# Performance work log

Hardware: AMD Instinct MI355X
Metric: run time of the kernel (lower is better)

The kernel has to match this reference:

```python
import jax, jax.numpy as jnp
import numpy as np

B, N, F, D, H, L, K = 128, 128, 13, 256, 8, 8, 10
FF = 2 * D  # FFN / hidden width
HEAD = D // H


def setup_inputs() -> dict:
    key = jax.random.key(0)
    ks = iter(jax.random.split(key, 64))
    def nrm(shape, scale=0.02):
        return jax.random.normal(next(ks), shape, dtype=jnp.float32) * scale
    return {
        "input_features": jax.random.normal(next(ks), (B, N, F), dtype=jnp.float32),
        "input_points": jax.random.normal(next(ks), (B, N, 2), dtype=jnp.float32),
        "input_mask": jnp.ones((B, N, 1), dtype=jnp.float32),
        "input_time": jax.random.uniform(next(ks), (B, 1), dtype=jnp.float32),
        # get_encoding: Dense(2D, gelu) -> Dense(D, gelu)
        "enc_w1": nrm((F, FF)), "enc_b1": jnp.zeros((FF,), jnp.float32),
        "enc_w2": nrm((FF, D)), "enc_b2": jnp.zeros((D,), jnp.float32),
        # FourierProjection MLP (no bias, swish)
        "four_w1": nrm((D, FF)), "four_w2": nrm((FF, D)),
        # FiLM time projection (no bias)
        "time_w": nrm((D, FF)),
        # local KNN MLPs: round 0 input 2*F, round 1 input 2*D
        "loc1_w1": nrm((2 * F, FF)), "loc1_b1": jnp.zeros((FF,), jnp.float32),
        "loc1_w2": nrm((FF, D)), "loc1_b2": jnp.zeros((D,), jnp.float32),
        "loc2_w1": nrm((2 * D, FF)), "loc2_b1": jnp.zeros((FF,), jnp.float32),
        "loc2_w2": nrm((FF, D)), "loc2_b2": jnp.zeros((D,), jnp.float32),
        # transformer encoder layers, stacked over L
        "qkv_w": nrm((L, D, 3 * D)), "qkv_b": jnp.zeros((L, 3 * D), jnp.float32),
        "out_w": nrm((L, D, D)), "out_b": jnp.zeros((L, D), jnp.float32),
        "ln1_g": jnp.ones((L, D), jnp.float32), "ln1_b": jnp.zeros((L, D), jnp.float32),
        "ff1_w": nrm((L, D, FF)), "ff1_b": jnp.zeros((L, FF), jnp.float32),
        "ff2_w": nrm((L, FF, D)), "ff2_b": jnp.zeros((L, D), jnp.float32),
        "gamma": jnp.full((L, D), 1e-5, dtype=jnp.float32),
        "ln2_g": jnp.ones((L, D), jnp.float32), "ln2_b": jnp.zeros((L, D), jnp.float32),
    }


def _ln(x, g, b, eps=1e-5):
    m = jnp.mean(x, axis=-1, keepdims=True)
    v = jnp.var(x, axis=-1, keepdims=True)
    return (x - m) * jax.lax.rsqrt(v + eps) * g + b


def _fourier(t, w1, w2):
    # t: (B,1) -> (B,D)
    half = D // 2
    emb = np.log(10000.0) / (half - 1)
    freq = jnp.exp(-emb * jnp.arange(half, dtype=jnp.float32))
    angle = t * freq[None, :] * 1000.0  # (B, half)
    e = jnp.concatenate([jnp.sin(angle), jnp.cos(angle)], axis=-1)
    e = jax.nn.silu(e @ w1)
    return jax.nn.silu(e @ w2)


def _get_neighbors(points, feats, w1, b1, w2, b2):
    # points: (B,N,P), feats: (B,N,C) -> (B,N,D)
    r = jnp.sum(points * points, axis=-1)  # (B,N)
    d = r[:, :, None] - 2.0 * jnp.einsum('bnp,bmp->bnm', points, points) + r[:, None, :]
    _, idx = jax.lax.top_k(-d, K + 1)
    idx = idx[:, :, 1:]  # drop self, (B,N,K)
    knn = jax.vmap(lambda f, i: f[i])(feats, idx)  # (B,N,K,C)
    center = jnp.broadcast_to(feats[:, :, None, :], knn.shape)
    local = jnp.concatenate([knn - center, center], axis=-1)  # (B,N,K,2C)
    local = jax.nn.gelu(local @ w1 + b1)
    local = jax.nn.gelu(local @ w2 + b2)
    return jnp.mean(local, axis=2)


def _mha(x, mask, wqkv, bqkv, wo, bo):
    Bx, Nx, _ = x.shape
    qkv = x @ wqkv + bqkv
    q, k, v = jnp.split(qkv, 3, axis=-1)
    def heads(t):
        return t.reshape(Bx, Nx, H, HEAD).transpose(0, 2, 1, 3)
    q, k, v = heads(q), heads(k), heads(v)
    scores = jnp.einsum('bhqd,bhkd->bhqk', q, k) * (1.0 / np.sqrt(HEAD))
    keep = mask[:, None, None, :, 0] > 0  # (B,1,1,N)
    scores = jnp.where(keep, scores, -1e9)
    a = jax.nn.softmax(scores, axis=-1)
    o = jnp.einsum('bhqk,bhkd->bhqd', a, v).transpose(0, 2, 1, 3).reshape(Bx, Nx, D)
    return o @ wo + bo


def _pet(input_features, input_points, input_mask, input_time,
         enc_w1, enc_b1, enc_w2, enc_b2, four_w1, four_w2, time_w,
         loc1_w1, loc1_b1, loc1_w2, loc1_b2, loc2_w1, loc2_b1, loc2_w2, loc2_b2,
         qkv_w, qkv_b, out_w, out_b, ln1_g, ln1_b, ff1_w, ff1_b, ff2_w, ff2_b,
         gamma, ln2_g, ln2_b):
    # feature encoding (RandomDrop is identity at eval / feature_drop=0)
    enc = jax.nn.gelu(input_features @ enc_w1 + enc_b1)
    enc = jax.nn.gelu(enc @ enc_w2 + enc_b2)  # (B,N,D)
    # FiLM time conditioning
    t = _fourier(input_time, four_w1, four_w2)  # (B,D)
    t = t[:, None, :] * input_mask  # (B,N,D)
    scale, shift = jnp.split(t @ time_w, 2, axis=-1)
    enc = enc * (1.0 + scale) + shift
    # local KNN aggregation
    coord_shift = 999.0 * (1.0 - input_mask)  # (B,N,1)
    points = input_points[:, :, :2]
    lf = _get_neighbors(coord_shift + points, input_features, loc1_w1, loc1_b1, loc1_w2, loc1_b2)
    lf = _get_neighbors(coord_shift + lf, lf, loc2_w1, loc2_b1, loc2_w2, loc2_b2)
    enc = enc + lf
    skip = enc
    x = enc
    for i in range(L):
        res = x
        a = _mha(x, input_mask, qkv_w[i], qkv_b[i], out_w[i], out_b[i])
        x = _ln(res + a, ln1_g[i], ln1_b[i])
        res = x
        h = jax.nn.gelu(x @ ff1_w[i] + ff1_b[i])
        h = h @ ff2_w[i] + ff2_b[i]
        h = h * gamma[i] * input_mask  # LayerScale with mask
        x = _ln(res + h, ln2_g[i], ln2_b[i])
    return x + skip


def reference(input_features, input_points, input_mask, input_time,
              enc_w1, enc_b1, enc_w2, enc_b2, four_w1, four_w2, time_w,
              loc1_w1, loc1_b1, loc1_w2, loc1_b2, loc2_w1, loc2_b1, loc2_w2, loc2_b2,
              qkv_w, qkv_b, out_w, out_b, ln1_g, ln1_b, ff1_w, ff1_b, ff2_w, ff2_b,
              gamma, ln2_g, ln2_b):
    return _pet(input_features, input_points, input_mask, input_time,
                enc_w1, enc_b1, enc_w2, enc_b2, four_w1, four_w2, time_w,
                loc1_w1, loc1_b1, loc1_w2, loc1_b2, loc2_w1, loc2_b1, loc2_w2, loc2_b2,
                qkv_w, qkv_b, out_w, out_b, ln1_g, ln1_b, ff1_w, ff1_b, ff2_w, ff2_b,
                gamma, ln2_g, ln2_b)
```

## Files before the change

kernel.cpp:

```cpp
#include <hip/hip_runtime.h>
#include <hip/hip_bf16.h>
#include <cmath>

#define DEV_INLINE __device__ __forceinline__

constexpr int Bn = 128;
constexpr int Nn = 128;
constexpr int Fn = 13;
constexpr int Dn = 256;
constexpr int Ln = 8;
constexpr int Kn = 10;
constexpr int FFn = 512;
constexpr int Tn = Bn * Nn;
constexpr int Rn = Tn * Kn;

typedef __attribute__((ext_vector_type(4))) float f32x4;
typedef __attribute__((ext_vector_type(8))) short bf16x8;
typedef unsigned short us;

__device__ float g_x[Tn * Dn];
__device__ float g_skip[Tn * Dn];
__device__ float g_big[Tn * Dn];
__device__ float g_u[Bn * FFn];
__device__ float g_r[Tn];
__device__ float g_pqbias[2048];
__device__ int   g_idx[Rn];
__device__ us g_bigb[Tn * 768];
__device__ us g_xb[Tn * Dn];
__device__ us g_attb[Tn * Dn];
__device__ us g_lf1b[Tn * Dn];
__device__ us g_pq[Tn * 1024];
__device__ us g_h2b[Rn * Dn];
__device__ us g_feat16[Tn * 32];
constexpr int OFF_ENC1 = 0;
constexpr int OFF_ENC2 = OFF_ENC1 + 512 * 32;
constexpr int OFF_W2A  = OFF_ENC2 + 256 * 512;
constexpr int OFF_W2B  = OFF_W2A + 256 * 512;
constexpr int OFF_PQ1  = OFF_W2B + 256 * 512;
constexpr int OFF_PQ2  = OFF_PQ1 + 1024 * 32;
constexpr int OFF_QKV  = OFF_PQ2 + 1024 * 256;
constexpr int OFF_OUT  = OFF_QKV + 8 * 768 * 256;
constexpr int OFF_FF1  = OFF_OUT + 8 * 256 * 256;
constexpr int OFF_FF2  = OFF_FF1 + 8 * 512 * 256;
constexpr int WT_TOTAL = OFF_FF2 + 8 * 256 * 512;
__device__ us g_wt[WT_TOTAL];

DEV_INLINE float gelu_f(float x) {
    float x2 = x * x;
    float m = x * fmaf(x2, -0.07135537f, -1.59576912f);
    float t = __expf(m);
    return x * __builtin_amdgcn_rcpf(1.f + t);
}
DEV_INLINE us f2b(float x) {
    __hip_bfloat16 h = __float2bfloat16(x);
    return *(us*)&h;
}
DEV_INLINE float blo(unsigned u) { return __uint_as_float(u << 16); }
DEV_INLINE float bhi(unsigned u) { return __uint_as_float(u & 0xFFFF0000u); }
DEV_INLINE unsigned pk2(float a, float b) {
    float2 f; f.x = a; f.y = b;
    __hip_bfloat162 h = __float22bfloat162_rn(f);
    return *(unsigned*)&h;
}

#define GLOAD16(gp, lp)                                                            \
    __builtin_amdgcn_global_load_lds(                                              \
        (const __attribute__((address_space(1))) unsigned int*)(gp),               \
        (__attribute__((address_space(3))) unsigned int*)(lp), 16, 0, 0)

constexpr int UP0 = 0;
constexpr int UP1 = UP0 + 16;
constexpr int UP2 = UP1 + 128;
constexpr int UP3 = UP2 + 128;
constexpr int UP4 = UP3 + 128;
constexpr int UP5 = UP4 + 1536;
constexpr int UP6 = UP5 + 512;
constexpr int UP7 = UP6 + 1024;
constexpr int UP8 = UP7 + 1024;
constexpr int UP9 = UP8 + 1024;
constexpr int UP10 = UP9 + 1024;
constexpr int UP11 = UP10 + 2048;
constexpr int UP12 = UP11 + 128;
constexpr int UPN = UP12 + 128;

DEV_INLINE void prep_seg(const float* __restrict__ src, us* __restrict__ dst,
                         int Kreal, int Kpad, int Nd, long sstride, long dstride,
                         int gx, int gy, int lb, int tid, float* tile) {
    int z = lb / (gx * gy);
    int rem = lb - z * gx * gy;
    int by = rem / gx, bx = rem - by * gx;
    const float* s = src + (size_t)z * sstride;
    us* d = dst + (size_t)z * dstride;
    int cn = tid & 31, rk = tid >> 5;
    int kbase = by * 32, nbase = bx * 32;
#pragma unroll
    for (int p = 0; p < 4; p++) {
        int k = kbase + p * 8 + rk;
        float v = (k < Kreal) ? s[(size_t)k * Nd + nbase + cn] : 0.f;
        tile[(p * 8 + rk) * 33 + cn] = v;
    }
    __syncthreads();
#pragma unroll
    for (int p = 0; p < 4; p++) {
        int nl = p * 8 + rk;
        d[(size_t)(nbase + nl) * Kpad + kbase + cn] = f2b(tile[cn * 33 + nl]);
    }
}

DEV_INLINE void prepPQ_seg(const float* __restrict__ w1, const float* __restrict__ b1,
                           us* __restrict__ dst, float* __restrict__ bdst,
                           int Kreal, int Kpad, int n, int tid) {
    for (int k = tid; k < Kpad; k += 256) {
        float v;
        if (n < 512) v = (k < Kreal) ? w1[(size_t)k * 512 + n] : 0.f;
        else {
            int m = n - 512;
            v = (k < Kreal) ? (w1[(size_t)(Kreal + k) * 512 + m] - w1[(size_t)k * 512 + m]) : 0.f;
        }
        dst[(size_t)n * Kpad + k] = f2b(v);
    }
    if (tid == 0) bdst[n] = (n < 512) ? 0.f : b1[n - 512];
}

__global__ __launch_bounds__(256) void k_uprep(
    const float* __restrict__ enc_w1, const float* __restrict__ enc_w2,
    const float* __restrict__ l1w2, const float* __restrict__ l2w2,
    const float* __restrict__ qkv_w, const float* __restrict__ out_w,
    const float* __restrict__ ff1w, const float* __restrict__ ff2w,
    const float* __restrict__ l1w1, const float* __restrict__ l1b1,
    const float* __restrict__ l2w1, const float* __restrict__ l2b1,
    const float* __restrict__ feat, const float* __restrict__ tin,
    const float* __restrict__ four_w1, const float* __restrict__ four_w2,
    const float* __restrict__ time_w, const float* __restrict__ pts,
    const float* __restrict__ mask,
    us* __restrict__ wt, float* __restrict__ pqbias, us* __restrict__ fp,
    float* __restrict__ u, int* __restrict__ idx) {
    __shared__ float shmem[1056];
    int b = blockIdx.x, tid = threadIdx.x;
    if (b < UP1) {
        prep_seg(enc_w1, wt + OFF_ENC1, 13, 32, 512, 0, 0, 16, 1, b - UP0, tid, shmem);
    } else if (b < UP2) {
        prep_seg(enc_w2, wt + OFF_ENC2, 512, 512, 256, 0, 0, 8, 16, b - UP1, tid, shmem);
    } else if (b < UP3) {
        prep_seg(l1w2, wt + OFF_W2A, 512, 512, 256, 0, 0, 8, 16, b - UP2, tid, shmem);
    } else if (b < UP4) {
        prep_seg(l2w2, wt + OFF_W2B, 512, 512, 256, 0, 0, 8, 16, b - UP3, tid, shmem);
    } else if (b < UP5) {
        prep_seg(qkv_w, wt + OFF_QKV, 256, 256, 768, 256 * 768, 768 * 256, 24, 8, b - UP4, tid, shmem);
    } else if (b < UP6) {
        prep_seg(out_w, wt + OFF_OUT, 256, 256, 256, 256 * 256, 256 * 256, 8, 8, b - UP5, tid, shmem);
    } else if (b < UP7) {
        prep_seg(ff1w, wt + OFF_FF1, 256, 256, 512, 256 * 512, 512 * 256, 16, 8, b - UP6, tid, shmem);
    } else if (b < UP8) {
        prep_seg(ff2w, wt + OFF_FF2, 512, 512, 256, 512 * 256, 256 * 512, 8, 16, b - UP7, tid, shmem);
    } else if (b < UP9) {
        prepPQ_seg(l1w1, l1b1, wt + OFF_PQ1, pqbias, 13, 32, b - UP8, tid);
    } else if (b < UP10) {
        prepPQ_seg(l2w1, l2b1, wt + OFF_PQ2, pqbias + 1024, 256, 256, b - UP9, tid);
    } else if (b < UP11) {
        int gid = (b - UP10) * 256 + tid;
        int t = gid >> 5, c = gid & 31;
        fp[gid] = (c < Fn) ? f2b(feat[(size_t)t * Fn + c]) : (us)0;
    } else if (b < UP12) {
        float* e = shmem; float* e1 = shmem + 256; float* t2 = shmem + 768;
        int bb = b - UP11;
        float tv = tin[bb];
        if (tid < 128) {
            const float emb = 0.07252236513366287f;
            float fr = expf(-emb * (float)tid);
            float ang = tv * fr * 1000.f;
            e[tid] = sinf(ang);
            e[tid + 128] = cosf(ang);
        }
        __syncthreads();
        for (int j = tid; j < 512; j += 256) {
            float s = 0.f;
            for (int i = 0; i < 256; i++) s += e[i] * four_w1[(size_t)i * 512 + j];
            e1[j] = s / (1.f + expf(-s));
        }
        __syncthreads();
        {
            float s = 0.f;
            for (int i = 0; i < 512; i++) s += e1[i] * four_w2[(size_t)i * 256 + tid];
            t2[tid] = s / (1.f + expf(-s));
        }
        __syncthreads();
        for (int j = tid; j < 512; j += 256) {
            float s = 0.f;
            for (int i = 0; i < 256; i++) s += t2[i] * time_w[(size_t)i * 512 + j];
            u[(size_t)bb * 512 + j] = s;
        }
    } else {
        float* px = shmem; float* py = shmem + 128; float* rr = shmem + 256;
        int bb = b - UP12;
        if (tid < 128) {
            int n = tid;
            float shift = 999.f * (1.f - mask[bb * Nn + n]);
            float x = pts[(size_t)(bb * Nn + n) * 2 + 0] + shift;
            float y = pts[(size_t)(bb * Nn + n) * 2 + 1] + shift;
            px[n] = x; py[n] = y; rr[n] = x * x + y * y;
        }
        __syncthreads();
        if (tid < 128) {
            int n = tid;
            float x = px[n], y = py[n], rn = rr[n];
            float bd[Kn + 1]; int bi[Kn + 1];
#pragma unroll
            for (int j = 0; j <= Kn; j++) { bd[j] = 3.4e38f; bi[j] = -1; }
            for (int m = 0; m < Nn; m++) {
                float d = rn - 2.f * (x * px[m] + y * py[m]) + rr[m];
                if (d < bd[Kn]) {
                    int j = Kn;
                    while (j > 0 && d < bd[j - 1]) { bd[j] = bd[j - 1]; bi[j] = bi[j - 1]; j--; }
                    bd[j] = d; bi[j] = m;
                }
            }
            for (int j = 1; j <= Kn; j++) idx[(size_t)(bb * Nn + n) * Kn + j - 1] = bi[j];
        }
    }
}

template <int EPI, bool OBF>
__global__ __launch_bounds__(256) void k_mg2(const us* __restrict__ A,
                                             const us* __restrict__ Bt,
                                             const float* __restrict__ bias,
                                             void* __restrict__ Cp,
                                             int Kd, int Nd) {
    __shared__ __align__(16) us As[128 * 32];
    __shared__ __align__(16) us Bs[128 * 32];
    int tid = threadIdx.x;
    int m0 = blockIdx.y << 7, n0 = blockIdx.x << 7;
    int wave = tid >> 6, lane = tid & 63;
    int wm = (wave & 1) << 6, wn = (wave >> 1) << 6;
    int lm = lane & 15, quad = lane >> 4;
    int r0 = (wave << 5) + (lane >> 2);
    int colu = (((lane & 3) ^ ((lane >> 2) & 3)) << 3);
    const us* pa0 = A + (size_t)(m0 + r0) * Kd + colu;
    const us* pa1 = A + (size_t)(m0 + r0 + 16) * Kd + colu;
    const us* pb0 = Bt + (size_t)(n0 + r0) * Kd + colu;
    const us* pb1 = Bt + (size_t)(n0 + r0 + 16) * Kd + colu;
    auto lAs = (__attribute__((address_space(3))) us*)As;
    auto lBs = (__attribute__((address_space(3))) us*)Bs;
    int lbase = wave << 10;
    int fcol = ((quad ^ (lm & 3)) << 3);
    f32x4 acc[4][4] = {};
    for (int k0 = 0; k0 < Kd; k0 += 32) {
        __syncthreads();
        GLOAD16(pa0 + k0, lAs + lbase);
        GLOAD16(pa1 + k0, lAs + lbase + 512);
        GLOAD16(pb0 + k0, lBs + lbase);
        GLOAD16(pb1 + k0, lBs + lbase + 512);
        __syncthreads();
        bf16x8 afr[4], bfr[4];
#pragma unroll
        for (int i = 0; i < 4; i++) {
            afr[i] = *(const bf16x8*)&As[(wm + i * 16 + lm) * 32 + fcol];
            bfr[i] = *(const bf16x8*)&Bs[(wn + i * 16 + lm) * 32 + fcol];
        }
#pragma unroll
        for (int mf = 0; mf < 4; mf++)
#pragma unroll
            for (int nf = 0; nf < 4; nf++)
                acc[mf][nf] = __builtin_amdgcn_mfma_f32_16x16x32_bf16(afr[mf], bfr[nf], acc[mf][nf], 0, 0, 0);
    }
    float bvs[4];
#pragma unroll
    for (int nf = 0; nf < 4; nf++) bvs[nf] = bias[n0 + wn + nf * 16 + lm];
#pragma unroll
    for (int mf = 0; mf < 4; mf++) {
#pragma unroll
        for (int r = 0; r < 4; r++) {
            size_t row = (size_t)(m0 + wm + mf * 16 + (quad << 2) + r);
#pragma unroll
            for (int nf = 0; nf < 4; nf++) {
                float v = acc[mf][nf][r] + bvs[nf];
                if (EPI == 1) v = gelu_f(v);
                size_t ci = row * Nd + n0 + wn + nf * 16 + lm;
                if constexpr (OBF) ((us*)Cp)[ci] = f2b(v);
                else ((float*)Cp)[ci] = v;
            }
        }
    }
}

template <bool PM, bool FINAL>
__global__ __launch_bounds__(512) void k_mgln(const us* __restrict__ A,
                                              const us* __restrict__ Bt,
                                              const float* __restrict__ bias,
                                              const float* __restrict__ res,
                                              const float* __restrict__ gamma,
                                              const float* __restrict__ mask,
                                              const float* __restrict__ lng,
                                              const float* __restrict__ lnb,
                                              const float* __restrict__ skip,
                                              float* __restrict__ xout,
                                              us* __restrict__ xbout,
                                              float* __restrict__ finout,
                                              int Kd) {
    __shared__ __align__(16) us As[128 * 32];
    __shared__ __align__(16) us Bs[256 * 32];
    __shared__ float2 part[4][128];
    __shared__ float2 stat[128];
    int tid = threadIdx.x;
    int m0 = blockIdx.x << 7;
    int wave = tid >> 6, lane = tid & 63;
    int wm = (wave & 1) << 6, wn = (wave >> 1) << 6;
    int grp = wave >> 1;
    int lm = lane & 15, quad = lane >> 4;
    int ar = (wave << 4) + (lane >> 2);
    int br = (wave << 5) + (lane >> 2);
    int colu = (((lane & 3) ^ ((lane >> 2) & 3)) << 3);
    const us* pa = A + (size_t)(m0 + ar) * Kd + colu;
    const us* pb0 = Bt + (size_t)br * Kd + colu;
    const us* pb1 = Bt + (size_t)(br + 16) * Kd + colu;
    auto lAs = (__attribute__((address_space(3))) us*)As;
    auto lBs = (__attribute__((address_space(3))) us*)Bs;
    int fcol = ((quad ^ (lm & 3)) << 3);
    f32x4 acc[4][4] = {};
    for (int k0 = 0; k0 < Kd; k0 += 32) {
        __syncthreads();
        GLOAD16(pa + k0, lAs + (wave << 9));
        GLOAD16(pb0 + k0, lBs + (wave << 10));
        GLOAD16(pb1 + k0, lBs + (wave << 10) + 512);
        __syncthreads();
        bf16x8 afr[4], bfr[4];
#pragma unroll
        for (int i = 0; i < 4; i++) {
            afr[i] = *(const bf16x8*)&As[(wm + i * 16 + lm) * 32 + fcol];
            bfr[i] = *(const bf16x8*)&Bs[(wn + i * 16 + lm) * 32 + fcol];
        }
#pragma unroll
        for (int mf = 0; mf < 4; mf++)
#pragma unroll
            for (int nf = 0; nf < 4; nf++)
                acc[mf][nf] = __builtin_amdgcn_mfma_f32_16x16x32_bf16(afr[mf], bfr[nf], acc[mf][nf], 0, 0, 0);
    }
    float bvs[4], gms[4];
#pragma unroll
    for (int nf = 0; nf < 4; nf++) {
        int col = wn + nf * 16 + lm;
        bvs[nf] = bias[col];
        if (PM) gms[nf] = gamma[col];
    }
#pragma unroll
    for (int mf = 0; mf < 4; mf++) {
#pragma unroll
        for (int r = 0; r < 4; r++) {
            int rowl = wm + mf * 16 + (quad << 2) + r;
            size_t row = (size_t)(m0 + rowl);
            float mrow = PM ? mask[row] : 0.f;
            float s1 = 0.f, s2 = 0.f;
#pragma unroll
            for (int nf = 0; nf < 4; nf++) {
                int col = wn + nf * 16 + lm;
                float rv = res[row * 256 + col];
                float v = acc[mf][nf][r] + bvs[nf];
                v = PM ? fmaf(v * gms[nf], mrow, rv) : rv + v;
                acc[mf][nf][r] = v;
                s1 += v; s2 += v * v;
            }
            s1 += __shfl_xor(s1, 1, 64); s2 += __shfl_xor(s2, 1, 64);
            s1 += __shfl_xor(s1, 2, 64); s2 += __shfl_xor(s2, 2, 64);
            s1 += __shfl_xor(s1, 4, 64); s2 += __shfl_xor(s2, 4, 64);
            s1 += __shfl_xor(s1, 8, 64); s2 += __shfl_xor(s2, 8, 64);
            if (lm == 0) { float2 p; p.x = s1; p.y = s2; part[grp][rowl] = p; }
        }
    }
    __syncthreads();
    if (tid < 128) {
        float2 p0 = part[0][tid], p1 = part[1][tid], p2 = part[2][tid], p3 = part[3][tid];
        float s = p0.x + p1.x + p2.x + p3.x;
        float q = p0.y + p1.y + p2.y + p3.y;
        float mean = s * (1.f / 256.f);
        float var = q * (1.f / 256.f) - mean * mean;
        float2 st; st.x = mean; st.y = rsqrtf(var + 1e-5f);
        stat[tid] = st;
    }
    __syncthreads();
    float gvs[4], bts[4];
#pragma unroll
    for (int nf = 0; nf < 4; nf++) {
        int col = wn + nf * 16 + lm;
        gvs[nf] = lng[col];
        bts[nf] = lnb[col];
    }
#pragma unroll
    for (int mf = 0; mf < 4; mf++) {
#pragma unroll
        for (int r = 0; r < 4; r++) {
            int rowl = wm + mf * 16 + (quad << 2) + r;
            size_t row = (size_t)(m0 + rowl);
            float2 st = stat[rowl];
#pragma unroll
            for (int nf = 0; nf < 4; nf++) {
                int col = wn + nf * 16 + lm;
                float nv = fmaf((acc[mf][nf][r] - st.x) * st.y, gvs[nf], bts[nf]);
                xout[row * 256 + col] = nv;
                xbout[row * 256 + col] = f2b(nv);
                if (FINAL) finout[row * 256 + col] = nv + skip[row * 256 + col];
            }
        }
    }
}

__global__ __launch_bounds__(512) void k_knng(const us* __restrict__ pq,
                                              const int* __restrict__ idx,
                                              const us* __restrict__ Bt,
                                              const float* __restrict__ bias,
                                              us* __restrict__ h2b) {
    __shared__ __align__(16) us As[128 * 64];
    __shared__ __align__(16) us Bs[256 * 64];
    int tid = threadIdx.x;
    int m0 = blockIdx.x << 7;
    int wave = tid >> 6, lane = tid & 63;
    int wm = (wave & 1) << 6, wn = (wave >> 1) << 6;
    int lm = lane & 15, quad = lane >> 4;
    int arow = tid >> 2, acolu = (tid & 3) << 4;
    int asw = arow & 7;
    int ablk0 = ((tid & 3) << 1) ^ asw, ablk1 = (((tid & 3) << 1) + 1) ^ asw;
    int r = m0 + arow;
    int tok = r / 10;
    int nb = idx[r];
    int prow = (tok & ~127) + nb;
    const us* Pp = pq + (size_t)prow * 1024 + acolu;
    const us* Qp = pq + (size_t)tok * 1024 + 512 + acolu;
    int brow = (wave << 5) + (lane >> 3);
    int bcol = (((lane & 7) ^ (lane >> 3)) << 3);
    const us* pb = Bt + (size_t)brow * 512 + bcol;
    auto lBs = (__attribute__((address_space(3))) us*)Bs;
    int lbase = wave << 11;
    int fsw = lm & 7;
    f32x4 acc[4][4] = {};
    for (int k0 = 0; k0 < 512; k0 += 64) {
        uint4 pv0 = *(const uint4*)(Pp + k0);
        uint4 pv1 = *(const uint4*)(Pp + k0 + 8);
        uint4 qv0 = *(const uint4*)(Qp + k0);
        uint4 qv1 = *(const uint4*)(Qp + k0 + 8);
        uint4 h0, h1;
        h0.x = pk2(gelu_f(blo(pv0.x) + blo(qv0.x)), gelu_f(bhi(pv0.x) + bhi(qv0.x)));
        h0.y = pk2(gelu_f(blo(pv0.y) + blo(qv0.y)), gelu_f(bhi(pv0.y) + bhi(qv0.y)));
        h0.z = pk2(gelu_f(blo(pv0.z) + blo(qv0.z)), gelu_f(bhi(pv0.z) + bhi(qv0.z)));
        h0.w = pk2(gelu_f(blo(pv0.w) + blo(qv0.w)), gelu_f(bhi(pv0.w) + bhi(qv0.w)));
        h1.x = pk2(gelu_f(blo(pv1.x) + blo(qv1.x)), gelu_f(bhi(pv1.x) + bhi(qv1.x)));
        h1.y = pk2(gelu_f(blo(pv1.y) + blo(qv1.y)), gelu_f(bhi(pv1.y) + bhi(qv1.y)));
        h1.z = pk2(gelu_f(blo(pv1.z) + blo(qv1.z)), gelu_f(bhi(pv1.z) + bhi(qv1.z)));
        h1.w = pk2(gelu_f(blo(pv1.w) + blo(qv1.w)), gelu_f(bhi(pv1.w) + bhi(qv1.w)));
        __syncthreads();
        GLOAD16(pb + k0, lBs + lbase);
        GLOAD16(pb + k0 + 8 * 512, lBs + lbase + 512);
        GLOAD16(pb + k0 + 16 * 512, lBs + lbase + 1024);
        GLOAD16(pb + k0 + 24 * 512, lBs + lbase + 1536);
        *(uint4*)&As[arow * 64 + (ablk0 << 3)] = h0;
        *(uint4*)&As[arow * 64 + (ablk1 << 3)] = h1;
        __syncthreads();
#pragma unroll
        for (int sub = 0; sub < 2; sub++) {
            int lblk = (sub << 2) + quad;
            int fcol = ((lblk ^ fsw) << 3);
            bf16x8 afr[4], bfr[4];
#pragma unroll
            for (int i = 0; i < 4; i++) {
                afr[i] = *(const bf16x8*)&As[(wm + i * 16 + lm) * 64 + fcol];
                bfr[i] = *(const bf16x8*)&Bs[(wn + i * 16 + lm) * 64 + fcol];
            }
#pragma unroll
            for (int mf = 0; mf < 4; mf++)
#pragma unroll
                for (int nf = 0; nf < 4; nf++)
                    acc[mf][nf] = __builtin_amdgcn_mfma_f32_16x16x32_bf16(afr[mf], bfr[nf], acc[mf][nf], 0, 0, 0);
        }
    }
    float bvs[4];
#pragma unroll
    for (int nf = 0; nf < 4; nf++) bvs[nf] = bias[wn + nf * 16 + lm];
#pragma unroll
    for (int mf = 0; mf < 4; mf++) {
#pragma unroll
        for (int rr = 0; rr < 4; rr++) {
            size_t row = (size_t)(m0 + wm + mf * 16 + (quad << 2) + rr);
#pragma unroll
            for (int nf = 0; nf < 4; nf++) {
                float v = gelu_f(acc[mf][nf][rr] + bvs[nf]);
                h2b[row * 256 + wn + nf * 16 + lm] = f2b(v);
            }
        }
    }
}

__global__ __launch_bounds__(64) void k_mean1s(const us* __restrict__ h2b,
                                               const float* __restrict__ mask,
                                               us* __restrict__ lfb,
                                               float* __restrict__ big,
                                               float* __restrict__ r) {
    int t = blockIdx.x, lane = threadIdx.x;
    int c = lane << 2;
    const us* p = h2b + (size_t)t * Kn * 256 + c;
    float s0 = 0.f, s1 = 0.f, s2 = 0.f, s3 = 0.f;
#pragma unroll
    for (int k = 0; k < Kn; k++) {
        uint2 v = *(const uint2*)(p + k * 256);
        s0 += blo(v.x); s1 += bhi(v.x);
        s2 += blo(v.y); s3 += bhi(v.y);
    }
    s0 *= 0.1f; s1 *= 0.1f; s2 *= 0.1f; s3 *= 0.1f;
    uint2 ob; ob.x = pk2(s0, s1); ob.y = pk2(s2, s3);
    *(uint2*)&lfb[(size_t)t * 256 + c] = ob;
    float sh = 999.f * (1.f - mask[t]);
    float4 w; w.x = s0 + sh; w.y = s1 + sh; w.z = s2 + sh; w.w = s3 + sh;
    *(float4*)&big[(size_t)t * 256 + c] = w;
    float sq = w.x * w.x + w.y * w.y + w.z * w.z + w.w * w.w;
#pragma unroll
    for (int off = 32; off; off >>= 1) sq += __shfl_xor(sq, off, 64);
    if (lane == 0) r[t] = sq;
}

__global__ __launch_bounds__(256) void k_dtop(const float* __restrict__ big,
                                              const float* __restrict__ r,
                                              int* __restrict__ idx) {
    __shared__ float Dm[128][132];
    __shared__ float At[16][132];
    int b = blockIdx.x, tid = threadIdx.x;
    int tx = tid & 15, ty = tid >> 4;
    const float* A = big + (size_t)b * Nn * Dn;
    float acc[8][8] = {};
    int srow = tid >> 1, sc8 = (tid & 1) << 3;
    for (int k0 = 0; k0 < 256; k0 += 16) {
        float4 v0 = *(const float4*)&A[(size_t)srow * 256 + k0 + sc8];
        float4 v1 = *(const float4*)&A[(size_t)srow * 256 + k0 + sc8 + 4];
        __syncthreads();
        At[sc8 + 0][srow] = v0.x; At[sc8 + 1][srow] = v0.y;
        At[sc8 + 2][srow] = v0.z; At[sc8 + 3][srow] = v0.w;
        At[sc8 + 4][srow] = v1.x; At[sc8 + 5][srow] = v1.y;
        At[sc8 + 6][srow] = v1.z; At[sc8 + 7][srow] = v1.w;
        __syncthreads();
#pragma unroll
        for (int kk = 0; kk < 16; kk++) {
            float av[8], bv[8];
#pragma unroll
            for (int i = 0; i < 8; i++) av[i] = At[kk][ty * 8 + i];
#pragma unroll
            for (int j = 0; j < 8; j++) bv[j] = At[kk][tx * 8 + j];
#pragma unroll
            for (int i = 0; i < 8; i++)
#pragma unroll
                for (int j = 0; j < 8; j++) acc[i][j] += av[i] * bv[j];
        }
    }
    __syncthreads();
#pragma unroll
    for (int i = 0; i < 8; i++) {
        int n = ty * 8 + i;
        float rn = r[b * Nn + n];
#pragma unroll
        for (int j = 0; j < 8; j++) {
            int m = tx * 8 + j;
            Dm[n][m] = rn - 2.f * acc[i][j] + r[b * Nn + m];
        }
    }
    __syncthreads();
    if (tid < 128) {
        int n = tid;
        float bd[Kn + 1]; int bi[Kn + 1];
#pragma unroll
        for (int j = 0; j <= Kn; j++) { bd[j] = 3.4e38f; bi[j] = -1; }
        for (int m = 0; m < Nn; m++) {
            float d = Dm[n][m];
            if (d < bd[Kn]) {
                int j = Kn;
                while (j > 0 && d < bd[j - 1]) { bd[j] = bd[j - 1]; bi[j] = bi[j - 1]; j--; }
                bd[j] = d; bi[j] = m;
            }
        }
        for (int j = 1; j <= Kn; j++) idx[(size_t)(b * Nn + n) * Kn + j - 1] = bi[j];
    }
}

__global__ __launch_bounds__(256) void k_meanc(const us* __restrict__ h2b,
                                               const float* __restrict__ u,
                                               const float* __restrict__ mask,
                                               float* __restrict__ x,
                                               float* __restrict__ skip,
                                               us* __restrict__ xb) {
    int t = blockIdx.x, c = threadIdx.x;
    const us* p = h2b + (size_t)t * Kn * 256 + c;
    float s = 0.f;
#pragma unroll
    for (int k = 0; k < Kn; k++) s += blo((unsigned)p[k * 256]);
    s *= 0.1f;
    int b = t >> 7;
    float m = mask[t];
    float xv = x[(size_t)t * Dn + c];
    float sc = u[(size_t)b * 512 + c];
    float sh = u[(size_t)b * 512 + 256 + c];
    float v = xv * (1.f + m * sc) + m * sh + s;
    x[(size_t)t * Dn + c] = v;
    skip[(size_t)t * Dn + c] = v;
    xb[(size_t)t * Dn + c] = f2b(v);
}

__global__ __launch_bounds__(256) void k_attn(const us* __restrict__ qkv,
                                              const float* __restrict__ mask,
                                              us* __restrict__ outp) {
    __shared__ __align__(16) us Qs[128 * 40];
    __shared__ __align__(16) us Ks[128 * 40];
    __shared__ __align__(16) us Vt[32 * 136];
    __shared__ __align__(16) us Ps[128 * 136];
    __shared__ float msk[128];
    int bh = blockIdx.x;
    int b = bh >> 3, h = bh & 7;
    int tid = threadIdx.x;
    int wave = tid >> 6, lane = tid & 63;
    int lm = lane & 15, quad = lane >> 4;
    int wm = wave << 5;
    {
        int row = tid >> 1, off = (tid & 1) << 4;
        const us* rp = qkv + (size_t)(b * 128 + row) * 768 + h * 32 + off;
        *(uint4*)&Qs[row * 40 + off] = *(const uint4*)(rp);
        *(uint4*)&Qs[row * 40 + off + 8] = *(const uint4*)(rp + 8);
        *(uint4*)&Ks[row * 40 + off] = *(const uint4*)(rp + 256);
        *(uint4*)&Ks[row * 40 + off + 8] = *(const uint4*)(rp + 264);
        union { uint4 u[2]; us s[16]; } tv;
        tv.u[0] = *(const uint4*)(rp + 512);
        tv.u[1] = *(const uint4*)(rp + 520);
#pragma unroll
        for (int j = 0; j < 16; j++) Vt[(off + j) * 136 + row] = tv.s[j];
        if (tid < 128) msk[tid] = mask[b * 128 + tid];
    }
    __syncthreads();
    f32x4 acc[2][8] = {};
    {
        bf16x8 aq[2];
#pragma unroll
        for (int mf = 0; mf < 2; mf++)
            aq[mf] = *(const bf16x8*)&Qs[(wm + mf * 16 + lm) * 40 + (quad << 3)];
#pragma unroll
        for (int nf = 0; nf < 8; nf++) {
            bf16x8 bk = *(const bf16x8*)&Ks[(nf * 16 + lm) * 40 + (quad << 3)];
            acc[0][nf] = __builtin_amdgcn_mfma_f32_16x16x32_bf16(aq[0], bk, acc[0][nf], 0, 0, 0);
            acc[1][nf] = __builtin_amdgcn_mfma_f32_16x16x32_bf16(aq[1], bk, acc[1][nf], 0, 0, 0);
        }
    }
    {
        const float sc = 0.17677669529663687f;
        float mkc[8];
#pragma unroll
        for (int nf = 0; nf < 8; nf++) mkc[nf] = msk[nf * 16 + lm];
#pragma unroll
        for (int mf = 0; mf < 2; mf++) {
#pragma unroll
            for (int nf = 0; nf < 8; nf++)
#pragma unroll
                for (int r = 0; r < 4; r++) {
                    float s = acc[mf][nf][r];
                    acc[mf][nf][r] = mkc[nf] > 0.f ? s * sc : -1.0e9f;
                }
#pragma unroll
            for (int r = 0; r < 4; r++) {
                float m = acc[mf][0][r];
#pragma unroll
                for (int nf = 1; nf < 8; nf++) m = fmaxf(m, acc[mf][nf][r]);
                m = fmaxf(m, __shfl_xor(m, 1, 64));
                m = fmaxf(m, __shfl_xor(m, 2, 64));
                m = fmaxf(m, __shfl_xor(m, 4, 64));
                m = fmaxf(m, __shfl_xor(m, 8, 64));
                float s = 0.f;
#pragma unroll
                for (int nf = 0; nf < 8; nf++) {
                    float p = __expf(acc[mf][nf][r] - m);
                    acc[mf][nf][r] = p;
                    s += p;
                }
                s += __shfl_xor(s, 1, 64);
                s += __shfl_xor(s, 2, 64);
                s += __shfl_xor(s, 4, 64);
                s += __shfl_xor(s, 8, 64);
                float linv = __builtin_amdgcn_rcpf(s);
                int prow = wm + mf * 16 + (quad << 2) + r;
#pragma unroll
                for (int nf = 0; nf < 8; nf++)
                    Ps[prow * 136 + nf * 16 + lm] = f2b(acc[mf][nf][r] * linv);
            }
        }
    }
    __syncthreads();
    f32x4 oacc[2][2] = {};
    for (int kt = 0; kt < 4; kt++) {
        bf16x8 ap[2], bv[2];
#pragma unroll
        for (int mf = 0; mf < 2; mf++)
            ap[mf] = *(const bf16x8*)&Ps[(wm + mf * 16 + lm) * 136 + kt * 32 + (quad << 3)];
#pragma unroll
        for (int nf = 0; nf < 2; nf++)
            bv[nf] = *(const bf16x8*)&Vt[(nf * 16 + lm) * 136 + kt * 32 + (quad << 3)];
#pragma unroll
        for (int mf = 0; mf < 2; mf++)
#pragma unroll
            for (int nf = 0; nf < 2; nf++)
                oacc[mf][nf] = __builtin_amdgcn_mfma_f32_16x16x32_bf16(ap[mf], bv[nf], oacc[mf][nf], 0, 0, 0);
    }
#pragma unroll
    for (int mf = 0; mf < 2; mf++)
#pragma unroll
        for (int r = 0; r < 4; r++) {
            int row = wm + mf * 16 + (quad << 2) + r;
#pragma unroll
            for (int nf = 0; nf < 2; nf++)
                outp[(size_t)(b * 128 + row) * 256 + h * 32 + nf * 16 + lm] = f2b(oacc[mf][nf][r]);
        }
}

extern "C" void kernel_launch(void* const* d_in, const int* in_sizes, int n_in,
                              void* d_out, int out_size, void* d_ws, size_t ws_size,
                              hipStream_t stream) {
    (void)in_sizes; (void)n_in; (void)out_size; (void)d_ws; (void)ws_size;
    const float* f_feat = (const float*)d_in[0];
    const float* f_pts  = (const float*)d_in[1];
    const float* f_mask = (const float*)d_in[2];
    const float* f_time = (const float*)d_in[3];
    const float* enc_w1 = (const float*)d_in[4];
    const float* enc_b1 = (const float*)d_in[5];
    const float* enc_w2 = (const float*)d_in[6];
    const float* enc_b2 = (const float*)d_in[7];
    const float* four_w1 = (const float*)d_in[8];
    const float* four_w2 = (const float*)d_in[9];
    const float* time_w = (const float*)d_in[10];
    const float* l1w1 = (const float*)d_in[11];
    const float* l1b1 = (const float*)d_in[12];
    const float* l1w2 = (const float*)d_in[13];
    const float* l1b2 = (const float*)d_in[14];
    const float* l2w1 = (const float*)d_in[15];
    const float* l2b1 = (const float*)d_in[16];
    const float* l2w2 = (const float*)d_in[17];
    const float* l2b2 = (const float*)d_in[18];
    const float* qkv_w = (const float*)d_in[19];
    const float* qkv_b = (const float*)d_in[20];
    const float* out_w = (const float*)d_in[21];
    const float* out_b = (const float*)d_in[22];
    const float* ln1g = (const float*)d_in[23];
    const float* ln1b = (const float*)d_in[24];
    const float* ff1w = (const float*)d_in[25];
    const float* ff1b = (const float*)d_in[26];
    const float* ff2w = (const float*)d_in[27];
    const float* ff2b = (const float*)d_in[28];
    const float* gam  = (const float*)d_in[29];
    const float* ln2g = (const float*)d_in[30];
    const float* ln2b = (const float*)d_in[31];
    float* out = (float*)d_out;

    float *x, *skip, *big, *u, *r, *pqbias;
    int* idx;
    us *bigb, *xb, *attb, *lf1b, *pq, *h2b, *feat16, *wt;
    hipGetSymbolAddress((void**)&x,    HIP_SYMBOL(g_x));
    hipGetSymbolAddress((void**)&skip, HIP_SYMBOL(g_skip));
    hipGetSymbolAddress((void**)&big,  HIP_SYMBOL(g_big));
    hipGetSymbolAddress((void**)&u,    HIP_SYMBOL(g_u));
    hipGetSymbolAddress((void**)&r,    HIP_SYMBOL(g_r));
    hipGetSymbolAddress((void**)&pqbias, HIP_SYMBOL(g_pqbias));
    hipGetSymbolAddress((void**)&idx,  HIP_SYMBOL(g_idx));
    hipGetSymbolAddress((void**)&bigb, HIP_SYMBOL(g_bigb));
    hipGetSymbolAddress((void**)&xb,   HIP_SYMBOL(g_xb));
    hipGetSymbolAddress((void**)&attb, HIP_SYMBOL(g_attb));
    hipGetSymbolAddress((void**)&lf1b, HIP_SYMBOL(g_lf1b));
    hipGetSymbolAddress((void**)&pq,   HIP_SYMBOL(g_pq));
    hipGetSymbolAddress((void**)&h2b,  HIP_SYMBOL(g_h2b));
    hipGetSymbolAddress((void**)&feat16, HIP_SYMBOL(g_feat16));
    hipGetSymbolAddress((void**)&wt,   HIP_SYMBOL(g_wt));

    k_uprep<<<UPN, 256, 0, stream>>>(
        enc_w1, enc_w2, l1w2, l2w2, qkv_w, out_w, ff1w, ff2w,
        l1w1, l1b1, l2w1, l2b1, f_feat, f_time, four_w1, four_w2, time_w,
        f_pts, f_mask, wt, pqbias, feat16, u, idx);

    k_mg2<1, true><<<dim3(4, 128), 256, 0, stream>>>(feat16, wt + OFF_ENC1, enc_b1, bigb, 32, 512);
    k_mg2<1, false><<<dim3(2, 128), 256, 0, stream>>>(bigb, wt + OFF_ENC2, enc_b2, x, 512, 256);
    k_mg2<0, true><<<dim3(8, 128), 256, 0, stream>>>(feat16, wt + OFF_PQ1, pqbias, pq, 32, 1024);
    k_knng<<<Rn / 128, 512, 0, stream>>>(pq, idx, wt + OFF_W2A, l1b2, h2b);
    k_mean1s<<<Tn, 64, 0, stream>>>(h2b, f_mask, lf1b, big, r);
    k_dtop<<<Bn, 256, 0, stream>>>(big, r, idx);
    k_mg2<0, true><<<dim3(8, 128), 256, 0, stream>>>(lf1b, wt + OFF_PQ2, pqbias + 1024, pq, 256, 1024);
    k_knng<<<Rn / 128, 512, 0, stream>>>(pq, idx, wt + OFF_W2B, l2b2, h2b);
    k_meanc<<<Tn, 256, 0, stream>>>(h2b, u, f_mask, x, skip, xb);
    for (int l = 0; l < Ln; l++) {
        k_mg2<0, true><<<dim3(6, 128), 256, 0, stream>>>(
            xb, wt + OFF_QKV + (size_t)l * 768 * 256, qkv_b + l * 768, bigb, 256, 768);
        k_attn<<<Bn * 8, 256, 0, stream>>>(bigb, f_mask, attb);
        k_mgln<false, false><<<128, 512, 0, stream>>>(
            attb, wt + OFF_OUT + (size_t)l * 256 * 256, out_b + l * 256,
            x, nullptr, f_mask, ln1g + l * Dn, ln1b + l * Dn, nullptr, x, xb, nullptr, 256);
        k_mg2<1, true><<<dim3(4, 128), 256, 0, stream>>>(
            xb, wt + OFF_FF1 + (size_t)l * 512 * 256, ff1b + l * 512, bigb, 256, 512);
        if (l < Ln - 1)
            k_mgln<true, false><<<128, 512, 0, stream>>>(
                bigb, wt + OFF_FF2 + (size_t)l * 256 * 512, ff2b + l * 256,
                x, gam + l * Dn, f_mask, ln2g + l * Dn, ln2b + l * Dn, nullptr, x, xb, nullptr, 512);
        else
            k_mgln<true, true><<<128, 512, 0, stream>>>(
                bigb, wt + OFF_FF2 + (size_t)l * 256 * 512, ff2b + l * 256,
                x, gam + l * Dn, f_mask, ln2g + l * Dn, ln2b + l * Dn, skip, x, xb, out, 512);
    }
}
```

Baseline: 1.572 ms.

## Keep residual stream in bf16 only and split kNN distance/top-k kernels

The fp32 residual copy of x is removed: the fused GEMM+LayerNorm kernels now read the residual from the bf16 activation buffer and write the normalized result back to it in place. This cuts global memory reads and writes in every layer. In exchange, the residual is rounded to bf16 at each of the 16 LayerNorm stages, which can accumulate error. Separately, the per-batch distance-plus-top-k kernel is split into a tiled distance GEMM spread over more blocks, which writes a global distance matrix, and a separate per-row top-k kernel.

```diff
diff --git a/kernel.cpp b/kernel.cpp
--- a/kernel.cpp
+++ b/kernel.cpp
@@ -21,6 +21,7 @@
 __device__ float g_x[Tn * Dn];
 __device__ float g_skip[Tn * Dn];
 __device__ float g_big[Tn * Dn];
+__device__ float g_dm[Tn * Nn];
 __device__ float g_u[Bn * FFn];
 __device__ float g_r[Tn];
 __device__ float g_pqbias[2048];
@@ -287,13 +288,12 @@
 __global__ __launch_bounds__(512) void k_mgln(const us* __restrict__ A,
                                               const us* __restrict__ Bt,
                                               const float* __restrict__ bias,
-                                              const float* __restrict__ res,
+                                              const us* __restrict__ res,
                                               const float* __restrict__ gamma,
                                               const float* __restrict__ mask,
                                               const float* __restrict__ lng,
                                               const float* __restrict__ lnb,
                                               const float* __restrict__ skip,
-                                              float* __restrict__ xout,
                                               us* __restrict__ xbout,
                                               float* __restrict__ finout,
                                               int Kd) {
@@ -353,7 +353,7 @@
 #pragma unroll
             for (int nf = 0; nf < 4; nf++) {
                 int col = wn + nf * 16 + lm;
-                float rv = res[row * 256 + col];
+                float rv = blo((unsigned)res[row * 256 + col]);
                 float v = acc[mf][nf][r] + bvs[nf];
                 v = PM ? fmaf(v * gms[nf], mrow, rv) : rv + v;
                 acc[mf][nf][r] = v;
@@ -395,9 +395,8 @@
             for (int nf = 0; nf < 4; nf++) {
                 int col = wn + nf * 16 + lm;
                 float nv = fmaf((acc[mf][nf][r] - st.x) * st.y, gvs[nf], bts[nf]);
-                xout[row * 256 + col] = nv;
-                xbout[row * 256 + col] = f2b(nv);
                 if (FINAL) finout[row * 256 + col] = nv + skip[row * 256 + col];
+                else xbout[row * 256 + col] = f2b(nv);
             }
         }
     }
@@ -514,71 +513,70 @@
     if (lane == 0) r[t] = sq;
 }
 
-__global__ __launch_bounds__(256) void k_dtop(const float* __restrict__ big,
+__global__ __launch_bounds__(256) void k_dist(const float* __restrict__ fe,
                                               const float* __restrict__ r,
-                                              int* __restrict__ idx) {
-    __shared__ float Dm[128][132];
-    __shared__ float At[16][132];
-    int b = blockIdx.x, tid = threadIdx.x;
+                                              float* __restrict__ Dm) {
+    int b = blockIdx.z;
+    int m0 = blockIdx.x * 64, n0 = blockIdx.y * 64;
+    const float* A = fe + (size_t)b * Nn * Dn;
+    __shared__ float As[16][68];
+    __shared__ float Bs[16][68];
+    int tid = threadIdx.x;
     int tx = tid & 15, ty = tid >> 4;
-    const float* A = big + (size_t)b * Nn * Dn;
-    float acc[8][8] = {};
-    int srow = tid >> 1, sc8 = (tid & 1) << 3;
-    for (int k0 = 0; k0 < 256; k0 += 16) {
-        float4 v0 = *(const float4*)&A[(size_t)srow * 256 + k0 + sc8];
-        float4 v1 = *(const float4*)&A[(size_t)srow * 256 + k0 + sc8 + 4];
-        __syncthreads();
-        At[sc8 + 0][srow] = v0.x; At[sc8 + 1][srow] = v0.y;
-        At[sc8 + 2][srow] = v0.z; At[sc8 + 3][srow] = v0.w;
-        At[sc8 + 4][srow] = v1.x; At[sc8 + 5][srow] = v1.y;
-        At[sc8 + 6][srow] = v1.z; At[sc8 + 7][srow] = v1.w;
+    int ar = tid >> 2, ac = (tid & 3) << 2;
+    float acc[4][4] = {};
+    for (int k0 = 0; k0 < Dn; k0 += 16) {
+        float4 av = *(const float4*)&A[(size_t)(n0 + ar) * Dn + k0 + ac];
+        float4 bv = *(const float4*)&A[(size_t)(m0 + ar) * Dn + k0 + ac];
+        __syncthreads();
+        As[ac + 0][ar] = av.x; As[ac + 1][ar] = av.y; As[ac + 2][ar] = av.z; As[ac + 3][ar] = av.w;
+        Bs[ac + 0][ar] = bv.x; Bs[ac + 1][ar] = bv.y; Bs[ac + 2][ar] = bv.z; Bs[ac + 3][ar] = bv.w;
         __syncthreads();
 #pragma unroll
         for (int kk = 0; kk < 16; kk++) {
-            float av[8], bv[8];
-#pragma unroll
-            for (int i = 0; i < 8; i++) av[i] = At[kk][ty * 8 + i];
-#pragma unroll
-            for (int j = 0; j < 8; j++) bv[j] = At[kk][tx * 8 + j];
-#pragma unroll
-            for (int i = 0; i < 8; i++)
-#pragma unroll
-                for (int j = 0; j < 8; j++) acc[i][j] += av[i] * bv[j];
-        }
-    }
-    __syncthreads();
-#pragma unroll
-    for (int i = 0; i < 8; i++) {
-        int n = ty * 8 + i;
+            float4 a = *(const float4*)&As[kk][ty << 2];
+            float4 b2 = *(const float4*)&Bs[kk][tx << 2];
+            acc[0][0] += a.x * b2.x; acc[0][1] += a.x * b2.y; acc[0][2] += a.x * b2.z; acc[0][3] += a.x * b2.w;
+            acc[1][0] += a.y * b2.x; acc[1][1] += a.y * b2.y; acc[1][2] += a.y * b2.z; acc[1][3] += a.y * b2.w;
+            acc[2][0] += a.z * b2.x; acc[2][1] += a.z * b2.y; acc[2][2] += a.z * b2.z; acc[2][3] += a.z * b2.w;
+            acc[3][0] += a.w * b2.x; acc[3][1] += a.w * b2.y; acc[3][2] += a.w * b2.z; acc[3][3] += a.w * b2.w;
+        }
+    }
+    float4 rm = *(const float4*)&r[b * Nn + m0 + (tx << 2)];
+#pragma unroll
+    for (int i = 0; i < 4; i++) {
+        int n = n0 + (ty << 2) + i;
         float rn = r[b * Nn + n];
-#pragma unroll
-        for (int j = 0; j < 8; j++) {
-            int m = tx * 8 + j;
-            Dm[n][m] = rn - 2.f * acc[i][j] + r[b * Nn + m];
-        }
-    }
-    __syncthreads();
-    if (tid < 128) {
-        int n = tid;
-        float bd[Kn + 1]; int bi[Kn + 1];
-#pragma unroll
-        for (int j = 0; j <= Kn; j++) { bd[j] = 3.4e38f; bi[j] = -1; }
-        for (int m = 0; m < Nn; m++) {
-            float d = Dm[n][m];
-            if (d < bd[Kn]) {
-                int j = Kn;
-                while (j > 0 && d < bd[j - 1]) { bd[j] = bd[j - 1]; bi[j] = bi[j - 1]; j--; }
-                bd[j] = d; bi[j] = m;
-            }
-        }
-        for (int j = 1; j <= Kn; j++) idx[(size_t)(b * Nn + n) * Kn + j - 1] = bi[j];
-    }
+        float4 v;
+        v.x = rn - 2.f * acc[i][0] + rm.x;
+        v.y = rn - 2.f * acc[i][1] + rm.y;
+        v.z = rn - 2.f * acc[i][2] + rm.z;
+        v.w = rn - 2.f * acc[i][3] + rm.w;
+        *(float4*)&Dm[(size_t)b * Nn * Nn + (size_t)n * Nn + m0 + (tx << 2)] = v;
+    }
+}
+
+__global__ __launch_bounds__(128) void k_topkg(const float* __restrict__ Dm, int* __restrict__ idx) {
+    int b = blockIdx.x, n = threadIdx.x;
+    const float* row = Dm + (size_t)b * Nn * Nn + (size_t)n * Nn;
+    float bd[Kn + 1]; int bi[Kn + 1];
+#pragma unroll
+    for (int j = 0; j <= Kn; j++) { bd[j] = 3.4e38f; bi[j] = -1; }
+    for (int m = 0; m < Nn; m++) {
+        float d = row[m];
+        if (d < bd[Kn]) {
+            int j = Kn;
+            while (j > 0 && d < bd[j - 1]) { bd[j] = bd[j - 1]; bi[j] = bi[j - 1]; j--; }
+            bd[j] = d; bi[j] = m;
+        }
+    }
+    for (int j = 1; j <= Kn; j++) idx[(size_t)(b * Nn + n) * Kn + j - 1] = bi[j];
 }
 
 __global__ __launch_bounds__(256) void k_meanc(const us* __restrict__ h2b,
                                                const float* __restrict__ u,
                                                const float* __restrict__ mask,
-                                               float* __restrict__ x,
+                                               const float* __restrict__ x,
                                                float* __restrict__ skip,
                                                us* __restrict__ xb) {
     int t = blockIdx.x, c = threadIdx.x;
@@ -593,7 +591,6 @@
     float sc = u[(size_t)b * 512 + c];
     float sh = u[(size_t)b * 512 + 256 + c];
     float v = xv * (1.f + m * sc) + m * sh + s;
-    x[(size_t)t * Dn + c] = v;
     skip[(size_t)t * Dn + c] = v;
     xb[(size_t)t * Dn + c] = f2b(v);
 }
@@ -747,12 +744,13 @@
     const float* ln2b = (const float*)d_in[31];
     float* out = (float*)d_out;
 
-    float *x, *skip, *big, *u, *r, *pqbias;
+    float *x, *skip, *big, *dm, *u, *r, *pqbias;
     int* idx;
     us *bigb, *xb, *attb, *lf1b, *pq, *h2b, *feat16, *wt;
     hipGetSymbolAddress((void**)&x,    HIP_SYMBOL(g_x));
     hipGetSymbolAddress((void**)&skip, HIP_SYMBOL(g_skip));
     hipGetSymbolAddress((void**)&big,  HIP_SYMBOL(g_big));
+    hipGetSymbolAddress((void**)&dm,   HIP_SYMBOL(g_dm));
     hipGetSymbolAddress((void**)&u,    HIP_SYMBOL(g_u));
     hipGetSymbolAddress((void**)&r,    HIP_SYMBOL(g_r));
     hipGetSymbolAddress((void**)&pqbias, HIP_SYMBOL(g_pqbias));
@@ -776,7 +774,8 @@
     k_mg2<0, true><<<dim3(8, 128), 256, 0, stream>>>(feat16, wt + OFF_PQ1, pqbias, pq, 32, 1024);
     k_knng<<<Rn / 128, 512, 0, stream>>>(pq, idx, wt + OFF_W2A, l1b2, h2b);
     k_mean1s<<<Tn, 64, 0, stream>>>(h2b, f_mask, lf1b, big, r);
-    k_dtop<<<Bn, 256, 0, stream>>>(big, r, idx);
+    k_dist<<<dim3(2, 2, Bn), 256, 0, stream>>>(big, r, dm);
+    k_topkg<<<Bn, Nn, 0, stream>>>(dm, idx);
     k_mg2<0, true><<<dim3(8, 128), 256, 0, stream>>>(lf1b, wt + OFF_PQ2, pqbias + 1024, pq, 256, 1024);
     k_knng<<<Rn / 128, 512, 0, stream>>>(pq, idx, wt + OFF_W2B, l2b2, h2b);
     k_meanc<<<Tn, 256, 0, stream>>>(h2b, u, f_mask, x, skip, xb);
@@ -786,16 +785,16 @@
         k_attn<<<Bn * 8, 256, 0, stream>>>(bigb, f_mask, attb);
         k_mgln<false, false><<<128, 512, 0, stream>>>(
             attb, wt + OFF_OUT + (size_t)l * 256 * 256, out_b + l * 256,
-            x, nullptr, f_mask, ln1g + l * Dn, ln1b + l * Dn, nullptr, x, xb, nullptr, 256);
+            xb, nullptr, f_mask, ln1g + l * Dn, ln1b + l * Dn, nullptr, xb, nullptr, 256);
         k_mg2<1, true><<<dim3(4, 128), 256, 0, stream>>>(
             xb, wt + OFF_FF1 + (size_t)l * 512 * 256, ff1b + l * 512, bigb, 256, 512);
         if (l < Ln - 1)
             k_mgln<true, false><<<128, 512, 0, stream>>>(
                 bigb, wt + OFF_FF2 + (size_t)l * 256 * 512, ff2b + l * 256,
-                x, gam + l * Dn, f_mask, ln2g + l * Dn, ln2b + l * Dn, nullptr, x, xb, nullptr, 512);
+                xb, gam + l * Dn, f_mask, ln2g + l * Dn, ln2b + l * Dn, nullptr, xb, nullptr, 512);
         else
             k_mgln<true, true><<<128, 512, 0, stream>>>(
                 bigb, wt + OFF_FF2 + (size_t)l * 256 * 512, ff2b + l * 256,
-                x, gam + l * Dn, f_mask, ln2g + l * Dn, ln2b + l * Dn, skip, x, xb, out, 512);
-    }
-}
+                xb, gam + l * Dn, f_mask, ln2g + l * Dn, ln2b + l * Dn, skip, nullptr, out, 512);
+    }
+}
```

After: 1.511 ms. 3.9% less time.
